# Performance work log

Measured on AMD Instinct MI355X. Metric: run time of the kernel, lower is better.

The kernel has to match this reference:

```python
import jax, jax.numpy as jnp
import numpy as np

N = 40000      # nodes
E = 640000     # edges
D = 128        # input_dim == hidden_dim
G = 64         # graphs in batch


def _mk_linear(key, din, dout):
    kw, kb = jax.random.split(key)
    w = jax.random.normal(kw, (din, dout), jnp.float32) / np.sqrt(din)
    b = jax.random.normal(kb, (dout,), jnp.float32) * 0.01
    return w, b


def setup_inputs() -> dict:
    key = jax.random.key(0)
    ks = jax.random.split(key, 12)
    x = jax.random.normal(ks[0], (N, D), jnp.float32)
    edge_attr = jax.random.normal(ks[1], (E, D), jnp.float32)
    edge_index = jax.random.randint(ks[2], (2, E), 0, N, jnp.int32)
    batch = jnp.sort(jax.random.randint(ks[3], (N,), 0, G, jnp.int32))
    inp = {"x": x, "edge_attr": edge_attr, "edge_index": edge_index, "batch": batch}
    # 4 GINE layers, each with a 2-layer MLP (Linear-ReLU-Linear)
    for i in range(4):
        w1, b1 = _mk_linear(ks[4 + 2 * i], D, D)
        w2, b2 = _mk_linear(ks[5 + 2 * i], D, D)
        inp[f"w{i+1}_1"] = w1
        inp[f"b{i+1}_1"] = b1
        inp[f"w{i+1}_2"] = w2
        inp[f"b{i+1}_2"] = b2
    return inp


def _gine_layer(x, src, dst, edge_attr, w1, b1, w2, b2):
    # message: ReLU(x_src + edge_attr), scatter-sum into dst (PyG GINEConv, eps=0)
    msg = jax.nn.relu(x[src] + edge_attr)                      # [E, D]
    agg = jax.ops.segment_sum(msg, dst, num_segments=N)       # [N, D]
    h = x + agg                                                # (1+eps)*x + agg, eps=0
    h = jnp.maximum(h @ w1 + b1, 0.0) @ w2 + b2                # 2-layer MLP
    return h


def reference(x, edge_attr, edge_index, batch,
              w1_1, b1_1, w1_2, b1_2,
              w2_1, b2_1, w2_2, b2_2,
              w3_1, b3_1, w3_2, b3_2,
              w4_1, b4_1, w4_2, b4_2):
    src, dst = edge_index[0], edge_index[1]
    h = x
    params = [(w1_1, b1_1, w1_2, b1_2), (w2_1, b2_1, w2_2, b2_2),
              (w3_1, b3_1, w3_2, b3_2), (w4_1, b4_1, w4_2, b4_2)]
    for (w1, b1, w2, b2) in params:
        h = jax.nn.relu(_gine_layer(h, src, dst, edge_attr, w1, b1, w2, b2))
    # global mean pool over graphs
    sums = jax.ops.segment_sum(h, batch, num_segments=G)                 # [G, D]
    cnts = jax.ops.segment_sum(jnp.ones((N,), h.dtype), batch, num_segments=G)
    return sums / jnp.maximum(cnts, 1.0)[:, None]
```

## Files before the change

### kernel.cpp

```cpp
#include <hip/hip_runtime.h>

#define NN 40000
#define NE 640000
#define DD 128
#define NG 64

typedef float vf4 __attribute__((ext_vector_type(4)));
typedef unsigned short us4 __attribute__((ext_vector_type(4)));
typedef unsigned short us8 __attribute__((ext_vector_type(8)));
typedef short bf16x8 __attribute__((ext_vector_type(8)));
typedef float f32x4 __attribute__((ext_vector_type(4)));

__device__ inline unsigned short f2bf(float f) {
    unsigned int u = __float_as_uint(f);
    return (unsigned short)((u + 0x7fffu + ((u >> 16) & 1u)) >> 16);
}
__device__ inline float bf2f(unsigned short s) {
    return __uint_as_float((unsigned int)s << 16);
}

__global__ __launch_bounds__(256) void cvt_k(const float* __restrict__ ea,
                                             unsigned short* __restrict__ eb)
{
    size_t i = ((size_t)blockIdx.x * 256 + threadIdx.x) * 8;
    vf4 a = __builtin_nontemporal_load((const vf4*)(ea + i));
    vf4 b = __builtin_nontemporal_load((const vf4*)(ea + i + 4));
    us4 o0 = {f2bf(a.x), f2bf(a.y), f2bf(a.z), f2bf(a.w)};
    us4 o1 = {f2bf(b.x), f2bf(b.y), f2bf(b.z), f2bf(b.w)};
    *(us4*)(eb + i) = o0;
    *(us4*)(eb + i + 4) = o1;
}

__global__ __launch_bounds__(256) void wcvt_k(
    const float* __restrict__ m0, const float* __restrict__ m1,
    const float* __restrict__ m2, const float* __restrict__ m3,
    const float* __restrict__ m4, const float* __restrict__ m5,
    const float* __restrict__ m6, const float* __restrict__ m7,
    unsigned short* __restrict__ hi, unsigned short* __restrict__ lo)
{
    const float* ms[8] = {m0, m1, m2, m3, m4, m5, m6, m7};
    int mat = blockIdx.x >> 6;
    int idx = (blockIdx.x & 63) * 256 + threadIdx.x;
    float v = ms[mat][idx];
    int k = idx >> 7, n = idx & 127;
    unsigned short h = f2bf(v);
    size_t o = ((size_t)mat << 14) + (size_t)n * DD + k;
    hi[o] = h;
    lo[o] = f2bf(v - bf2f(h));
}

__global__ __launch_bounds__(256) void hist_k(const int* __restrict__ dst,
                                              int* __restrict__ cnt)
{
    int e = blockIdx.x * 256 + threadIdx.x;
    if (e < NE) atomicAdd(&cnt[dst[e]], 1);
}

__global__ __launch_bounds__(1024) void scan_k(const int* __restrict__ cnt,
                                               int* __restrict__ row_ptr,
                                               int* __restrict__ cursor)
{
    __shared__ int sm[1024];
    int t = threadIdx.x;
    int base = t * 40;
    int s = 0;
#pragma unroll 8
    for (int i = 0; i < 40; ++i) {
        int idx = base + i;
        if (idx < NN) s += cnt[idx];
    }
    sm[t] = s;
    __syncthreads();
    for (int off = 1; off < 1024; off <<= 1) {
        int x = (t >= off) ? sm[t - off] : 0;
        __syncthreads();
        sm[t] += x;
        __syncthreads();
    }
    int run = sm[t] - s;
#pragma unroll 8
    for (int i = 0; i < 40; ++i) {
        int idx = base + i;
        if (idx < NN) {
            row_ptr[idx] = run;
            cursor[idx] = run;
            run += cnt[idx];
        }
    }
    if (t == 1023) row_ptr[NN] = run;
}

__global__ __launch_bounds__(256) void fill_k(const int* __restrict__ src,
                                              const int* __restrict__ dst,
                                              int* __restrict__ cursor,
                                              int2* __restrict__ elist)
{
    int e = blockIdx.x * 256 + threadIdx.x;
    if (e < NE) {
        int d = dst[e];
        int pos = atomicAdd(&cursor[d], 1);
        elist[pos] = make_int2(src[e], e);
    }
}

__device__ inline void acc1(float4& acc, const unsigned short* __restrict__ hb,
                            const unsigned short* __restrict__ eb,
                            int s, int id, int lane)
{
    us4 xv = *(const us4*)(hb + (size_t)s * DD + lane * 4);
    us4 bv = *(const us4*)(eb + (size_t)id * DD + lane * 4);
    acc.x += fmaxf(bf2f(xv.x) + bf2f(bv.x), 0.f);
    acc.y += fmaxf(bf2f(xv.y) + bf2f(bv.y), 0.f);
    acc.z += fmaxf(bf2f(xv.z) + bf2f(bv.z), 0.f);
    acc.w += fmaxf(bf2f(xv.w) + bf2f(bv.w), 0.f);
}

__device__ inline void acc1_cvt(float4& acc, const unsigned short* __restrict__ hb,
                                const float* __restrict__ ea,
                                unsigned short* __restrict__ eb,
                                int s, int id, int lane)
{
    us4 xv = *(const us4*)(hb + (size_t)s * DD + lane * 4);
    const float4 ev = *(const float4*)(ea + (size_t)id * DD + lane * 4);
    us4 bv = {f2bf(ev.x), f2bf(ev.y), f2bf(ev.z), f2bf(ev.w)};
    *(us4*)(eb + (size_t)id * DD + lane * 4) = bv;
    acc.x += fmaxf(bf2f(xv.x) + bf2f(bv.x), 0.f);
    acc.y += fmaxf(bf2f(xv.y) + bf2f(bv.y), 0.f);
    acc.z += fmaxf(bf2f(xv.z) + bf2f(bv.z), 0.f);
    acc.w += fmaxf(bf2f(xv.w) + bf2f(bv.w), 0.f);
}

template <int L0>
__global__ __launch_bounds__(256) void gather_bf(
    const unsigned short* __restrict__ hb, const unsigned short* __restrict__ eb_r,
    const float* __restrict__ ea, unsigned short* __restrict__ eb_w,
    const int* __restrict__ row_ptr, const int2* __restrict__ elist,
    float* __restrict__ agg)
{
    int grp = blockIdx.x * 8 + (threadIdx.x >> 5);
    int lane = threadIdx.x & 31;
    if (grp >= NN) return;
    int beg = row_ptr[grp], end = row_ptr[grp + 1];

    float4 a0 = make_float4(0.f, 0.f, 0.f, 0.f);
    float4 a1 = make_float4(0.f, 0.f, 0.f, 0.f);
    float4 a2 = make_float4(0.f, 0.f, 0.f, 0.f);
    float4 a3 = make_float4(0.f, 0.f, 0.f, 0.f);
    int e = beg;
    for (; e + 4 <= end; e += 4) {
        int2 p0 = elist[e];
        int2 p1 = elist[e + 1];
        int2 p2 = elist[e + 2];
        int2 p3 = elist[e + 3];
        if (L0) {
            acc1_cvt(a0, hb, ea, eb_w, p0.x, p0.y, lane);
            acc1_cvt(a1, hb, ea, eb_w, p1.x, p1.y, lane);
            acc1_cvt(a2, hb, ea, eb_w, p2.x, p2.y, lane);
            acc1_cvt(a3, hb, ea, eb_w, p3.x, p3.y, lane);
        } else {
            acc1(a0, hb, eb_r, p0.x, p0.y, lane);
            acc1(a1, hb, eb_r, p1.x, p1.y, lane);
            acc1(a2, hb, eb_r, p2.x, p2.y, lane);
            acc1(a3, hb, eb_r, p3.x, p3.y, lane);
        }
    }
    for (; e < end; ++e) {
        int2 p0 = elist[e];
        if (L0) acc1_cvt(a0, hb, ea, eb_w, p0.x, p0.y, lane);
        else    acc1(a0, hb, eb_r, p0.x, p0.y, lane);
    }
    us4 sv = *(const us4*)(hb + (size_t)grp * DD + lane * 4);
    float4 o;
    o.x = bf2f(sv.x) + (a0.x + a1.x) + (a2.x + a3.x);
    o.y = bf2f(sv.y) + (a0.y + a1.y) + (a2.y + a3.y);
    o.z = bf2f(sv.z) + (a0.z + a1.z) + (a2.z + a3.z);
    o.w = bf2f(sv.w) + (a0.w + a1.w) + (a2.w + a3.w);
    *(float4*)(agg + (size_t)grp * DD + lane * 4) = o;
}

__device__ inline void acc1f(float4& acc, const float* __restrict__ h,
                             const float* __restrict__ ea,
                             int s, int id, int lane)
{
    const float4 xv = *(const float4*)(h + (size_t)s * DD + lane * 4);
    vf4 ev = __builtin_nontemporal_load((const vf4*)(ea + (size_t)id * DD + lane * 4));
    acc.x += fmaxf(xv.x + ev.x, 0.f);
    acc.y += fmaxf(xv.y + ev.y, 0.f);
    acc.z += fmaxf(xv.z + ev.z, 0.f);
    acc.w += fmaxf(xv.w + ev.w, 0.f);
}

__global__ __launch_bounds__(256) void gather_f32(
    const float* __restrict__ h, const float* __restrict__ ea,
    const int* __restrict__ row_ptr, const int2* __restrict__ elist,
    float* __restrict__ agg)
{
    int grp = blockIdx.x * 8 + (threadIdx.x >> 5);
    int lane = threadIdx.x & 31;
    if (grp >= NN) return;
    int beg = row_ptr[grp], end = row_ptr[grp + 1];

    float4 a0 = make_float4(0.f, 0.f, 0.f, 0.f);
    float4 a1 = make_float4(0.f, 0.f, 0.f, 0.f);
    float4 a2 = make_float4(0.f, 0.f, 0.f, 0.f);
    float4 a3 = make_float4(0.f, 0.f, 0.f, 0.f);
    int e = beg;
    for (; e + 4 <= end; e += 4) {
        int2 p0 = elist[e];
        int2 p1 = elist[e + 1];
        int2 p2 = elist[e + 2];
        int2 p3 = elist[e + 3];
        acc1f(a0, h, ea, p0.x, p0.y, lane);
        acc1f(a1, h, ea, p1.x, p1.y, lane);
        acc1f(a2, h, ea, p2.x, p2.y, lane);
        acc1f(a3, h, ea, p3.x, p3.y, lane);
    }
    for (; e < end; ++e) {
        int2 p0 = elist[e];
        acc1f(a0, h, ea, p0.x, p0.y, lane);
    }
    const float4 sv = *(const float4*)(h + (size_t)grp * DD + lane * 4);
    float4 o;
    o.x = sv.x + (a0.x + a1.x) + (a2.x + a3.x);
    o.y = sv.y + (a0.y + a1.y) + (a2.y + a3.y);
    o.z = sv.z + (a0.z + a1.z) + (a2.z + a3.z);
    o.w = sv.w + (a0.w + a1.w) + (a2.w + a3.w);
    *(float4*)(agg + (size_t)grp * DD + lane * 4) = o;
}

template <int OUT>
__global__ __launch_bounds__(256) void mlp_fused(
    const float* __restrict__ A,
    const unsigned short* __restrict__ W1h, const unsigned short* __restrict__ W1l,
    const float* __restrict__ b1v,
    const unsigned short* __restrict__ W2h, const unsigned short* __restrict__ W2l,
    const float* __restrict__ b2v,
    float* C, unsigned short* Cb)
{
    __shared__ __align__(16) char lds[96 * 1024];
    char* lAh = lds;
    char* lAl = lds + 16 * 1024;
    char* lBh = lds + 32 * 1024;
    char* lBl = lds + 64 * 1024;

    const int tid = threadIdx.x;
    const int m0 = blockIdx.x * 64;

    {
        const int row = tid >> 2;
        const int c0 = (tid & 3) * 32;
        const float* srcp = A + (size_t)(m0 + row) * DD + c0;
        const int base = row * 256 + c0 * 2;
        const int sw = (row & 7) << 4;
#pragma unroll
        for (int i = 0; i < 4; ++i) {
            float4 v0 = *(const float4*)(srcp + i * 8);
            float4 v1 = *(const float4*)(srcp + i * 8 + 4);
            float f[8] = {v0.x, v0.y, v0.z, v0.w, v1.x, v1.y, v1.z, v1.w};
            us8 hv, lv;
#pragma unroll
            for (int j = 0; j < 8; ++j) {
                unsigned short hb = f2bf(f[j]);
                hv[j] = hb;
                lv[j] = f2bf(f[j] - bf2f(hb));
            }
            const int off = (base + i * 16) ^ sw;
            *(us8*)(lAh + off) = hv;
            *(us8*)(lAl + off) = lv;
        }
    }
    const int wn = tid >> 1;
    const int wk0 = (tid & 1) * 64;
    const int wbase = wn * 256 + wk0 * 2;
    const int wsw = (wn & 7) << 4;
    {
        const unsigned short* sh = W1h + (size_t)wn * DD + wk0;
        const unsigned short* sl = W1l + (size_t)wn * DD + wk0;
#pragma unroll
        for (int i = 0; i < 8; ++i) {
            const int off = (wbase + i * 16) ^ wsw;
            *(us8*)(lBh + off) = *(const us8*)(sh + i * 8);
            *(us8*)(lBl + off) = *(const us8*)(sl + i * 8);
        }
    }
    __syncthreads();

    const int lane = tid & 63;
    const int wid = tid >> 6;
    const int lr = lane & 15;
    const int kg = lane >> 4;
    const int swr = (lr & 7) << 4;

    bf16x8 ah[4], al[4];
#pragma unroll
    for (int ks = 0; ks < 4; ++ks) {
        const int off = ((wid * 16 + lr) * 256 + ks * 64 + kg * 16) ^ swr;
        ah[ks] = *(const bf16x8*)(lAh + off);
        al[ks] = *(const bf16x8*)(lAl + off);
    }
    f32x4 acc[8];
#pragma unroll
    for (int nf = 0; nf < 8; ++nf) acc[nf] = (f32x4){0.f, 0.f, 0.f, 0.f};
#pragma unroll
    for (int nf = 0; nf < 8; ++nf) {
#pragma unroll
        for (int ks = 0; ks < 4; ++ks) {
            const int off = ((nf * 16 + lr) * 256 + ks * 64 + kg * 16) ^ swr;
            bf16x8 bh = *(const bf16x8*)(lBh + off);
            bf16x8 bl = *(const bf16x8*)(lBl + off);
            acc[nf] = __builtin_amdgcn_mfma_f32_16x16x32_bf16(ah[ks], bh, acc[nf], 0, 0, 0);
            acc[nf] = __builtin_amdgcn_mfma_f32_16x16x32_bf16(ah[ks], bl, acc[nf], 0, 0, 0);
            acc[nf] = __builtin_amdgcn_mfma_f32_16x16x32_bf16(al[ks], bh, acc[nf], 0, 0, 0);
        }
    }
    __syncthreads();

#pragma unroll
    for (int nf = 0; nf < 8; ++nf) {
        const int col = nf * 16 + lr;
        const float b = b1v[col];
#pragma unroll
        for (int r = 0; r < 4; ++r) {
            float u = fmaxf(acc[nf][r] + b, 0.0f);
            const int lrow = wid * 16 + kg * 4 + r;
            const int off = (lrow * 256 + col * 2) ^ ((lrow & 7) << 4);
            unsigned short hb = f2bf(u);
            *(unsigned short*)(lAh + off) = hb;
            *(unsigned short*)(lAl + off) = f2bf(u - bf2f(hb));
        }
    }
    {
        const unsigned short* sh = W2h + (size_t)wn * DD + wk0;
        const unsigned short* sl = W2l + (size_t)wn * DD + wk0;
#pragma unroll
        for (int i = 0; i < 8; ++i) {
            const int off = (wbase + i * 16) ^ wsw;
            *(us8*)(lBh + off) = *(const us8*)(sh + i * 8);
            *(us8*)(lBl + off) = *(const us8*)(sl + i * 8);
        }
    }
    __syncthreads();

#pragma unroll
    for (int ks = 0; ks < 4; ++ks) {
        const int off = ((wid * 16 + lr) * 256 + ks * 64 + kg * 16) ^ swr;
        ah[ks] = *(const bf16x8*)(lAh + off);
        al[ks] = *(const bf16x8*)(lAl + off);
    }
#pragma unroll
    for (int nf = 0; nf < 8; ++nf) acc[nf] = (f32x4){0.f, 0.f, 0.f, 0.f};
#pragma unroll
    for (int nf = 0; nf < 8; ++nf) {
#pragma unroll
        for (int ks = 0; ks < 4; ++ks) {
            const int off = ((nf * 16 + lr) * 256 + ks * 64 + kg * 16) ^ swr;
            bf16x8 bh = *(const bf16x8*)(lBh + off);
            bf16x8 bl = *(const bf16x8*)(lBl + off);
            acc[nf] = __builtin_amdgcn_mfma_f32_16x16x32_bf16(ah[ks], bh, acc[nf], 0, 0, 0);
            acc[nf] = __builtin_amdgcn_mfma_f32_16x16x32_bf16(ah[ks], bl, acc[nf], 0, 0, 0);
            acc[nf] = __builtin_amdgcn_mfma_f32_16x16x32_bf16(al[ks], bh, acc[nf], 0, 0, 0);
        }
    }
#pragma unroll
    for (int nf = 0; nf < 8; ++nf) {
        const int col = nf * 16 + lr;
        const float b = b2v[col];
        float v[4];
#pragma unroll
        for (int r = 0; r < 4; ++r) v[r] = fmaxf(acc[nf][r] + b, 0.0f);
        const size_t rbase = (size_t)(m0 + wid * 16 + kg * 4) * DD + col;
        if (OUT & 1) {
#pragma unroll
            for (int r = 0; r < 4; ++r) C[rbase + (size_t)r * DD] = v[r];
        }
        if (OUT & 2) {
#pragma unroll
            for (int r = 0; r < 4; ++r) Cb[rbase + (size_t)r * DD] = f2bf(v[r]);
        }
    }
}

__device__ inline void pool_flush(float* __restrict__ out, int g, int lane,
                                  const float4& acc)
{
    float* o = out + (size_t)g * DD + lane * 4;
    unsafeAtomicAdd(o + 0, acc.x);
    unsafeAtomicAdd(o + 1, acc.y);
    unsafeAtomicAdd(o + 2, acc.z);
    unsafeAtomicAdd(o + 3, acc.w);
}

__global__ __launch_bounds__(256) void pool_k(
    const float* __restrict__ h, const int* __restrict__ batch,
    float* __restrict__ out, int* __restrict__ cnt)
{
    int tid = blockIdx.x * 256 + threadIdx.x;
    int grp = tid >> 5;
    int lane = tid & 31;
    int n0 = grp * 16;
    if (n0 >= NN) return;
    int nend = min(n0 + 16, NN);

    float4 acc = make_float4(0.f, 0.f, 0.f, 0.f);
    int gprev = batch[n0];
    int crun = 0;
    for (int n = n0; n < nend; ++n) {
        int g = batch[n];
        if (g != gprev) {
            pool_flush(out, gprev, lane, acc);
            if (lane == 0) atomicAdd(cnt + gprev, crun);
            acc = make_float4(0.f, 0.f, 0.f, 0.f);
            crun = 0;
            gprev = g;
        }
        float4 v = *(const float4*)(h + (size_t)n * DD + lane * 4);
        acc.x += v.x; acc.y += v.y; acc.z += v.z; acc.w += v.w;
        ++crun;
    }
    pool_flush(out, gprev, lane, acc);
    if (lane == 0) atomicAdd(cnt + gprev, crun);
}

__global__ __launch_bounds__(256) void pool_div_k(float* __restrict__ out,
                                                  const int* __restrict__ cnt)
{
    int tid = blockIdx.x * 256 + threadIdx.x;
    if (tid >= NG * DD) return;
    int g = tid / DD;
    float c = fmaxf((float)cnt[g], 1.0f);
    out[tid] = out[tid] / c;
}

extern "C" void kernel_launch(void* const* d_in, const int* in_sizes, int n_in,
                              void* d_out, int out_size, void* d_ws, size_t ws_size,
                              hipStream_t stream)
{
    const float* x     = (const float*)d_in[0];
    const float* ea    = (const float*)d_in[1];
    const int*   ei    = (const int*)d_in[2];
    const int*   batch = (const int*)d_in[3];
    const float* w1[4], * b1[4], * w2[4], * b2[4];
    for (int l = 0; l < 4; ++l) {
        w1[l] = (const float*)d_in[4 + 4 * l];
        b1[l] = (const float*)d_in[5 + 4 * l];
        w2[l] = (const float*)d_in[6 + 4 * l];
        b2[l] = (const float*)d_in[7 + 4 * l];
    }

    const int* srcp = ei;
    const int* dstp = ei + NE;

    char* ws = (char*)d_ws;
    const size_t hbytes = (size_t)NN * DD * sizeof(float);
    float* agg = (float*)ws;
    float* hA  = (float*)(ws + hbytes);
    char*  p   = ws + 2 * hbytes;
    int*  cnt_node = (int*)p;           p += ((NN * 4 + 255) & ~255);
    int*  row_ptr  = (int*)p;           p += (((NN + 1) * 4 + 255) & ~255);
    int*  cursor   = (int*)p;           p += ((NN * 4 + 255) & ~255);
    int2* elist    = (int2*)p;          p += (((size_t)NE * 8 + 255) & ~255);
    int*  cntG     = (int*)p;           p += 256;
    unsigned short* wt_hi = (unsigned short*)p;  p += (size_t)8 * 16384 * 2;
    unsigned short* wt_lo = (unsigned short*)p;  p += (size_t)8 * 16384 * 2;
    unsigned short* hB = (unsigned short*)p;     p += (size_t)NN * DD * 2;
    unsigned short* ea_bf = (unsigned short*)p;
    const size_t need_bf = (size_t)(p - ws) + (size_t)NE * DD * 2;
    const bool use_bf = (ws_size >= need_bf);

    const int eblocks     = (NE + 255) / 256;
    const int gblocks     = (NN + 7) / 8;
    const int gemm_blocks = NN / 64;
    const int pool_blocks = ((NN / 16) * 32 + 255) / 256;

    if (use_bf)
        cvt_k<<<(size_t)NN * DD / 8 / 256, 256, 0, stream>>>(x, hB);
    wcvt_k<<<512, 256, 0, stream>>>(w1[0], w2[0], w1[1], w2[1],
                                    w1[2], w2[2], w1[3], w2[3], wt_hi, wt_lo);
    hipMemsetAsync(cnt_node, 0, NN * sizeof(int), stream);
    hist_k<<<eblocks, 256, 0, stream>>>(dstp, cnt_node);
    scan_k<<<1, 1024, 0, stream>>>(cnt_node, row_ptr, cursor);
    fill_k<<<eblocks, 256, 0, stream>>>(srcp, dstp, cursor, elist);

    if (use_bf) {
        for (int l = 0; l < 4; ++l) {
            if (l == 0)
                gather_bf<1><<<gblocks, 256, 0, stream>>>(hB, nullptr, ea, ea_bf,
                                                          row_ptr, elist, agg);
            else
                gather_bf<0><<<gblocks, 256, 0, stream>>>(hB, ea_bf, nullptr, nullptr,
                                                          row_ptr, elist, agg);
            const unsigned short* h1  = wt_hi + ((size_t)(2 * l) << 14);
            const unsigned short* lo1 = wt_lo + ((size_t)(2 * l) << 14);
            const unsigned short* h2  = wt_hi + ((size_t)(2 * l + 1) << 14);
            const unsigned short* lo2 = wt_lo + ((size_t)(2 * l + 1) << 14);
            if (l < 3)
                mlp_fused<2><<<gemm_blocks, 256, 0, stream>>>(
                    agg, h1, lo1, b1[l], h2, lo2, b2[l], nullptr, hB);
            else
                mlp_fused<1><<<gemm_blocks, 256, 0, stream>>>(
                    agg, h1, lo1, b1[l], h2, lo2, b2[l], hA, nullptr);
        }
    } else {
        const float* hcur = x;
        for (int l = 0; l < 4; ++l) {
            gather_f32<<<gblocks, 256, 0, stream>>>(hcur, ea, row_ptr, elist, agg);
            const unsigned short* h1  = wt_hi + ((size_t)(2 * l) << 14);
            const unsigned short* lo1 = wt_lo + ((size_t)(2 * l) << 14);
            const unsigned short* h2  = wt_hi + ((size_t)(2 * l + 1) << 14);
            const unsigned short* lo2 = wt_lo + ((size_t)(2 * l + 1) << 14);
            mlp_fused<1><<<gemm_blocks, 256, 0, stream>>>(
                agg, h1, lo1, b1[l], h2, lo2, b2[l], hA, nullptr);
            hcur = hA;
        }
    }

    hipMemsetAsync(d_out, 0, (size_t)NG * DD * sizeof(float), stream);
    hipMemsetAsync(cntG, 0, NG * sizeof(int), stream);
    pool_k<<<pool_blocks, 256, 0, stream>>>(hA, batch, (float*)d_out, cntG);
    pool_div_k<<<(NG * DD + 255) / 256, 256, 0, stream>>>((float*)d_out, cntG);
}
```

Measured before the change: 1.001 ms.

## Merge preamble kernels, halve MLP LDS for occupancy, vectorize scan, nontemporal edge loads

Merges the x conversion, weight conversion and degree histogram into one preamble launch to cut launch overhead. The fused MLP kernel now stages the weights in two 64-column halves, so LDS drops from 96 KB to 64 KB and launch bounds request two blocks per CU. This adds extra barriers and a second weight staging pass per GEMM. The scan kernel reads counts with int4 loads into registers, and edge-attribute loads in the gather become nontemporal to reduce cache pollution.

```diff
diff --git a/kernel.cpp b/kernel.cpp
--- a/kernel.cpp
+++ b/kernel.cpp
@@ -19,41 +19,46 @@
     return __uint_as_float((unsigned int)s << 16);
 }
 
-__global__ __launch_bounds__(256) void cvt_k(const float* __restrict__ ea,
-                                             unsigned short* __restrict__ eb)
-{
-    size_t i = ((size_t)blockIdx.x * 256 + threadIdx.x) * 8;
-    vf4 a = __builtin_nontemporal_load((const vf4*)(ea + i));
-    vf4 b = __builtin_nontemporal_load((const vf4*)(ea + i + 4));
-    us4 o0 = {f2bf(a.x), f2bf(a.y), f2bf(a.z), f2bf(a.w)};
-    us4 o1 = {f2bf(b.x), f2bf(b.y), f2bf(b.z), f2bf(b.w)};
-    *(us4*)(eb + i) = o0;
-    *(us4*)(eb + i + 4) = o1;
-}
-
-__global__ __launch_bounds__(256) void wcvt_k(
+#define PRE_CVT_BLKS  2500
+#define PRE_W_BLKS    512
+#define PRE_H_BLKS    2500
+#define PRE_BLOCKS    (PRE_CVT_BLKS + PRE_W_BLKS + PRE_H_BLKS)
+
+template <int USE_BF>
+__global__ __launch_bounds__(256) void preamble_k(
+    const float* __restrict__ x, unsigned short* __restrict__ hB,
     const float* __restrict__ m0, const float* __restrict__ m1,
     const float* __restrict__ m2, const float* __restrict__ m3,
     const float* __restrict__ m4, const float* __restrict__ m5,
     const float* __restrict__ m6, const float* __restrict__ m7,
-    unsigned short* __restrict__ hi, unsigned short* __restrict__ lo)
-{
-    const float* ms[8] = {m0, m1, m2, m3, m4, m5, m6, m7};
-    int mat = blockIdx.x >> 6;
-    int idx = (blockIdx.x & 63) * 256 + threadIdx.x;
-    float v = ms[mat][idx];
-    int k = idx >> 7, n = idx & 127;
-    unsigned short h = f2bf(v);
-    size_t o = ((size_t)mat << 14) + (size_t)n * DD + k;
-    hi[o] = h;
-    lo[o] = f2bf(v - bf2f(h));
-}
-
-__global__ __launch_bounds__(256) void hist_k(const int* __restrict__ dst,
-                                              int* __restrict__ cnt)
-{
-    int e = blockIdx.x * 256 + threadIdx.x;
-    if (e < NE) atomicAdd(&cnt[dst[e]], 1);
+    unsigned short* __restrict__ whi, unsigned short* __restrict__ wlo,
+    const int* __restrict__ dst, int* __restrict__ cnt)
+{
+    const int bid = blockIdx.x;
+    if (bid < PRE_CVT_BLKS) {
+        if (!USE_BF) return;
+        size_t i = ((size_t)bid * 256 + threadIdx.x) * 8;
+        vf4 a = __builtin_nontemporal_load((const vf4*)(x + i));
+        vf4 b = __builtin_nontemporal_load((const vf4*)(x + i + 4));
+        us4 o0 = {f2bf(a.x), f2bf(a.y), f2bf(a.z), f2bf(a.w)};
+        us4 o1 = {f2bf(b.x), f2bf(b.y), f2bf(b.z), f2bf(b.w)};
+        *(us4*)(hB + i) = o0;
+        *(us4*)(hB + i + 4) = o1;
+    } else if (bid < PRE_CVT_BLKS + PRE_W_BLKS) {
+        const float* ms[8] = {m0, m1, m2, m3, m4, m5, m6, m7};
+        int b = bid - PRE_CVT_BLKS;
+        int mat = b >> 6;
+        int idx = (b & 63) * 256 + threadIdx.x;
+        float v = ms[mat][idx];
+        int k = idx >> 7, n = idx & 127;
+        unsigned short h = f2bf(v);
+        size_t o = ((size_t)mat << 14) + (size_t)n * DD + k;
+        whi[o] = h;
+        wlo[o] = f2bf(v - bf2f(h));
+    } else {
+        int e = (bid - PRE_CVT_BLKS - PRE_W_BLKS) * 256 + threadIdx.x;
+        if (e < NE) atomicAdd(&cnt[dst[e]], 1);
+    }
 }
 
 __global__ __launch_bounds__(1024) void scan_k(const int* __restrict__ cnt,
@@ -63,12 +68,25 @@
     __shared__ int sm[1024];
     int t = threadIdx.x;
     int base = t * 40;
+    int4 buf[10];
+    if (base + 40 <= NN) {
+#pragma unroll
+        for (int i = 0; i < 10; ++i) buf[i] = ((const int4*)(cnt + base))[i];
+    } else {
+#pragma unroll
+        for (int i = 0; i < 10; ++i) {
+            int idx = base + i * 4;
+            int4 v = make_int4(0, 0, 0, 0);
+            if (idx + 0 < NN) v.x = cnt[idx + 0];
+            if (idx + 1 < NN) v.y = cnt[idx + 1];
+            if (idx + 2 < NN) v.z = cnt[idx + 2];
+            if (idx + 3 < NN) v.w = cnt[idx + 3];
+            buf[i] = v;
+        }
+    }
     int s = 0;
-#pragma unroll 8
-    for (int i = 0; i < 40; ++i) {
-        int idx = base + i;
-        if (idx < NN) s += cnt[idx];
-    }
+#pragma unroll
+    for (int i = 0; i < 10; ++i) s += buf[i].x + buf[i].y + buf[i].z + buf[i].w;
     sm[t] = s;
     __syncthreads();
     for (int off = 1; off < 1024; off <<= 1) {
@@ -78,14 +96,13 @@
         __syncthreads();
     }
     int run = sm[t] - s;
-#pragma unroll 8
-    for (int i = 0; i < 40; ++i) {
-        int idx = base + i;
-        if (idx < NN) {
-            row_ptr[idx] = run;
-            cursor[idx] = run;
-            run += cnt[idx];
-        }
+#pragma unroll
+    for (int i = 0; i < 10; ++i) {
+        int idx = base + i * 4;
+        if (idx + 0 < NN) { row_ptr[idx + 0] = run; cursor[idx + 0] = run; run += buf[i].x; }
+        if (idx + 1 < NN) { row_ptr[idx + 1] = run; cursor[idx + 1] = run; run += buf[i].y; }
+        if (idx + 2 < NN) { row_ptr[idx + 2] = run; cursor[idx + 2] = run; run += buf[i].z; }
+        if (idx + 3 < NN) { row_ptr[idx + 3] = run; cursor[idx + 3] = run; run += buf[i].w; }
     }
     if (t == 1023) row_ptr[NN] = run;
 }
@@ -108,7 +125,7 @@
                             int s, int id, int lane)
 {
     us4 xv = *(const us4*)(hb + (size_t)s * DD + lane * 4);
-    us4 bv = *(const us4*)(eb + (size_t)id * DD + lane * 4);
+    us4 bv = __builtin_nontemporal_load((const us4*)(eb + (size_t)id * DD + lane * 4));
     acc.x += fmaxf(bf2f(xv.x) + bf2f(bv.x), 0.f);
     acc.y += fmaxf(bf2f(xv.y) + bf2f(bv.y), 0.f);
     acc.z += fmaxf(bf2f(xv.z) + bf2f(bv.z), 0.f);
@@ -121,7 +138,7 @@
                                 int s, int id, int lane)
 {
     us4 xv = *(const us4*)(hb + (size_t)s * DD + lane * 4);
-    const float4 ev = *(const float4*)(ea + (size_t)id * DD + lane * 4);
+    vf4 ev = __builtin_nontemporal_load((const vf4*)(ea + (size_t)id * DD + lane * 4));
     us4 bv = {f2bf(ev.x), f2bf(ev.y), f2bf(ev.z), f2bf(ev.w)};
     *(us4*)(eb + (size_t)id * DD + lane * 4) = bv;
     acc.x += fmaxf(bf2f(xv.x) + bf2f(bv.x), 0.f);
@@ -229,7 +246,7 @@
 }
 
 template <int OUT>
-__global__ __launch_bounds__(256) void mlp_fused(
+__global__ __launch_bounds__(256, 2) void mlp_fused(
     const float* __restrict__ A,
     const unsigned short* __restrict__ W1h, const unsigned short* __restrict__ W1l,
     const float* __restrict__ b1v,
@@ -237,14 +254,30 @@
     const float* __restrict__ b2v,
     float* C, unsigned short* Cb)
 {
-    __shared__ __align__(16) char lds[96 * 1024];
+    __shared__ __align__(16) char lds[64 * 1024];
     char* lAh = lds;
     char* lAl = lds + 16 * 1024;
     char* lBh = lds + 32 * 1024;
-    char* lBl = lds + 64 * 1024;
+    char* lBl = lds + 48 * 1024;
 
     const int tid = threadIdx.x;
     const int m0 = blockIdx.x * 64;
+
+    const int wc  = tid >> 2;
+    const int wk0 = (tid & 3) * 32;
+    const int wbase = wc * 256 + wk0 * 2;
+    const int wsw = (wc & 7) << 4;
+    auto stageW = [&](const unsigned short* Wh_, const unsigned short* Wl_,
+                      int col0) {
+        const unsigned short* sh = Wh_ + (size_t)(col0 + wc) * DD + wk0;
+        const unsigned short* sl = Wl_ + (size_t)(col0 + wc) * DD + wk0;
+#pragma unroll
+        for (int i = 0; i < 4; ++i) {
+            const int off = (wbase + i * 16) ^ wsw;
+            *(us8*)(lBh + off) = *(const us8*)(sh + i * 8);
+            *(us8*)(lBl + off) = *(const us8*)(sl + i * 8);
+        }
+    };
 
     {
         const int row = tid >> 2;
@@ -269,20 +302,7 @@
             *(us8*)(lAl + off) = lv;
         }
     }
-    const int wn = tid >> 1;
-    const int wk0 = (tid & 1) * 64;
-    const int wbase = wn * 256 + wk0 * 2;
-    const int wsw = (wn & 7) << 4;
-    {
-        const unsigned short* sh = W1h + (size_t)wn * DD + wk0;
-        const unsigned short* sl = W1l + (size_t)wn * DD + wk0;
-#pragma unroll
-        for (int i = 0; i < 8; ++i) {
-            const int off = (wbase + i * 16) ^ wsw;
-            *(us8*)(lBh + off) = *(const us8*)(sh + i * 8);
-            *(us8*)(lBl + off) = *(const us8*)(sl + i * 8);
-        }
-    }
+    stageW(W1h, W1l, 0);
     __syncthreads();
 
     const int lane = tid & 63;
@@ -292,27 +312,38 @@
     const int swr = (lr & 7) << 4;
 
     bf16x8 ah[4], al[4];
-#pragma unroll
-    for (int ks = 0; ks < 4; ++ks) {
-        const int off = ((wid * 16 + lr) * 256 + ks * 64 + kg * 16) ^ swr;
-        ah[ks] = *(const bf16x8*)(lAh + off);
-        al[ks] = *(const bf16x8*)(lAl + off);
-    }
+    auto loadA = [&]() {
+#pragma unroll
+        for (int ks = 0; ks < 4; ++ks) {
+            const int off = ((wid * 16 + lr) * 256 + ks * 64 + kg * 16) ^ swr;
+            ah[ks] = *(const bf16x8*)(lAh + off);
+            al[ks] = *(const bf16x8*)(lAl + off);
+        }
+    };
     f32x4 acc[8];
+    auto mfma_half = [&](int ab) {
+#pragma unroll
+        for (int nfl = 0; nfl < 4; ++nfl) {
+#pragma unroll
+            for (int ks = 0; ks < 4; ++ks) {
+                const int off = ((nfl * 16 + lr) * 256 + ks * 64 + kg * 16) ^ swr;
+                bf16x8 bh = *(const bf16x8*)(lBh + off);
+                bf16x8 bl = *(const bf16x8*)(lBl + off);
+                acc[ab + nfl] = __builtin_amdgcn_mfma_f32_16x16x32_bf16(ah[ks], bh, acc[ab + nfl], 0, 0, 0);
+                acc[ab + nfl] = __builtin_amdgcn_mfma_f32_16x16x32_bf16(ah[ks], bl, acc[ab + nfl], 0, 0, 0);
+                acc[ab + nfl] = __builtin_amdgcn_mfma_f32_16x16x32_bf16(al[ks], bh, acc[ab + nfl], 0, 0, 0);
+            }
+        }
+    };
+
+    loadA();
 #pragma unroll
     for (int nf = 0; nf < 8; ++nf) acc[nf] = (f32x4){0.f, 0.f, 0.f, 0.f};
-#pragma unroll
-    for (int nf = 0; nf < 8; ++nf) {
-#pragma unroll
-        for (int ks = 0; ks < 4; ++ks) {
-            const int off = ((nf * 16 + lr) * 256 + ks * 64 + kg * 16) ^ swr;
-            bf16x8 bh = *(const bf16x8*)(lBh + off);
-            bf16x8 bl = *(const bf16x8*)(lBl + off);
-            acc[nf] = __builtin_amdgcn_mfma_f32_16x16x32_bf16(ah[ks], bh, acc[nf], 0, 0, 0);
-            acc[nf] = __builtin_amdgcn_mfma_f32_16x16x32_bf16(ah[ks], bl, acc[nf], 0, 0, 0);
-            acc[nf] = __builtin_amdgcn_mfma_f32_16x16x32_bf16(al[ks], bh, acc[nf], 0, 0, 0);
-        }
-    }
+    mfma_half(0);
+    __syncthreads();
+    stageW(W1h, W1l, 64);
+    __syncthreads();
+    mfma_half(4);
     __syncthreads();
 
 #pragma unroll
@@ -329,38 +360,18 @@
             *(unsigned short*)(lAl + off) = f2bf(u - bf2f(hb));
         }
     }
-    {
-        const unsigned short* sh = W2h + (size_t)wn * DD + wk0;
-        const unsigned short* sl = W2l + (size_t)wn * DD + wk0;
-#pragma unroll
-        for (int i = 0; i < 8; ++i) {
-            const int off = (wbase + i * 16) ^ wsw;
-            *(us8*)(lBh + off) = *(const us8*)(sh + i * 8);
-            *(us8*)(lBl + off) = *(const us8*)(sl + i * 8);
-        }
-    }
-    __syncthreads();
-
-#pragma unroll
-    for (int ks = 0; ks < 4; ++ks) {
-        const int off = ((wid * 16 + lr) * 256 + ks * 64 + kg * 16) ^ swr;
-        ah[ks] = *(const bf16x8*)(lAh + off);
-        al[ks] = *(const bf16x8*)(lAl + off);
-    }
+    stageW(W2h, W2l, 0);
+    __syncthreads();
+
+    loadA();
 #pragma unroll
     for (int nf = 0; nf < 8; ++nf) acc[nf] = (f32x4){0.f, 0.f, 0.f, 0.f};
-#pragma unroll
-    for (int nf = 0; nf < 8; ++nf) {
-#pragma unroll
-        for (int ks = 0; ks < 4; ++ks) {
-            const int off = ((nf * 16 + lr) * 256 + ks * 64 + kg * 16) ^ swr;
-            bf16x8 bh = *(const bf16x8*)(lBh + off);
-            bf16x8 bl = *(const bf16x8*)(lBl + off);
-            acc[nf] = __builtin_amdgcn_mfma_f32_16x16x32_bf16(ah[ks], bh, acc[nf], 0, 0, 0);
-            acc[nf] = __builtin_amdgcn_mfma_f32_16x16x32_bf16(ah[ks], bl, acc[nf], 0, 0, 0);
-            acc[nf] = __builtin_amdgcn_mfma_f32_16x16x32_bf16(al[ks], bh, acc[nf], 0, 0, 0);
-        }
-    }
+    mfma_half(0);
+    __syncthreads();
+    stageW(W2h, W2l, 64);
+    __syncthreads();
+    mfma_half(4);
+
 #pragma unroll
     for (int nf = 0; nf < 8; ++nf) {
         const int col = nf * 16 + lr;
@@ -472,12 +483,15 @@
     const int gemm_blocks = NN / 64;
     const int pool_blocks = ((NN / 16) * 32 + 255) / 256;
 
+    hipMemsetAsync(cnt_node, 0, NN * sizeof(int), stream);
     if (use_bf)
-        cvt_k<<<(size_t)NN * DD / 8 / 256, 256, 0, stream>>>(x, hB);
-    wcvt_k<<<512, 256, 0, stream>>>(w1[0], w2[0], w1[1], w2[1],
-                                    w1[2], w2[2], w1[3], w2[3], wt_hi, wt_lo);
-    hipMemsetAsync(cnt_node, 0, NN * sizeof(int), stream);
-    hist_k<<<eblocks, 256, 0, stream>>>(dstp, cnt_node);
+        preamble_k<1><<<PRE_BLOCKS, 256, 0, stream>>>(
+            x, hB, w1[0], w2[0], w1[1], w2[1], w1[2], w2[2], w1[3], w2[3],
+            wt_hi, wt_lo, dstp, cnt_node);
+    else
+        preamble_k<0><<<PRE_BLOCKS, 256, 0, stream>>>(
+            x, nullptr, w1[0], w2[0], w1[1], w2[1], w1[2], w2[2], w1[3], w2[3],
+            wt_hi, wt_lo, dstp, cnt_node);
     scan_k<<<1, 1024, 0, stream>>>(cnt_node, row_ptr, cursor);
     fill_k<<<eblocks, 256, 0, stream>>>(srcp, dstp, cursor, elist);
 
```

New measurement: 884.2 us. -11.6%, faster.
